# Optimization experiments

Measured on AMD Instinct MI355X. Metric: run time of the kernel, lower is better.

## Reference

```python
import jax, jax.numpy as jnp
import numpy as np

B, N, C, H = 2, 2048, 1024, 16
D = C // H          # head dim = 64
HID = 4 * C         # MLP hidden = 4096
LN_EPS = 1e-5
ROPE_BASE = 10000.0


def layernorm(x, g, b):
    mu = jnp.mean(x, axis=-1, keepdims=True)
    var = jnp.var(x, axis=-1, keepdims=True)
    return (x - mu) * jax.lax.rsqrt(var + LN_EPS) * g + b


def rotate_half(x):
    # interleaved pairs: (x0, x1) -> (-x1, x0), lucidrains rotary_embedding_torch style
    x = x.reshape(*x.shape[:-1], -1, 2)
    x1, x2 = x[..., 0], x[..., 1]
    return jnp.stack([-x2, x1], axis=-1).reshape(*x.shape[:-2], -1)


def rope_cos_sin(n, d, dtype):
    inv_freq = 1.0 / (ROPE_BASE ** (jnp.arange(0, d, 2, dtype=jnp.float32) / d))
    ang = jnp.arange(n, dtype=jnp.float32)[:, None] * inv_freq          # [N, D/2]
    ang = jnp.repeat(ang, 2, axis=-1)                                    # [N, D] interleaved
    return jnp.cos(ang).astype(dtype), jnp.sin(ang).astype(dtype)


def setup_inputs() -> dict:
    key = jax.random.key(0)
    ks = jax.random.split(key, 16)
    s = 0.02
    return {
        "x": jax.random.normal(ks[0], (B, N, C), jnp.float32),
        "ln1_g": jnp.ones((C,), jnp.float32),
        "ln1_b": jnp.zeros((C,), jnp.float32),
        "qkv_w": jax.random.normal(ks[1], (C, 3 * C), jnp.float32) * s,   # stored [in, out]
        "qkv_b": jnp.zeros((3 * C,), jnp.float32),
        "proj_w": jax.random.normal(ks[2], (C, C), jnp.float32) * s,
        "proj_b": jnp.zeros((C,), jnp.float32),
        "ln2_g": jnp.ones((C,), jnp.float32),
        "ln2_b": jnp.zeros((C,), jnp.float32),
        "fc1_w": jax.random.normal(ks[3], (C, HID), jnp.float32) * s,
        "fc1_b": jnp.zeros((HID,), jnp.float32),
        "ffn_ln_g": jnp.ones((HID,), jnp.float32),
        "ffn_ln_b": jnp.zeros((HID,), jnp.float32),
        "fc2_w": jax.random.normal(ks[4], (HID, C), jnp.float32) * s,
        "fc2_b": jnp.zeros((C,), jnp.float32),
    }


def reference(x, ln1_g, ln1_b, qkv_w, qkv_b, proj_w, proj_b,
              ln2_g, ln2_b, fc1_w, fc1_b, ffn_ln_g, ffn_ln_b, fc2_w, fc2_b):
    b, n, c = x.shape
    h, d = H, c // H
    scale = d ** -0.5

    # --- attention branch (pre-norm) ---
    hx = layernorm(x, ln1_g, ln1_b)
    qkv = hx @ qkv_w + qkv_b                                   # [B,N,3C]
    qkv = qkv.reshape(b, n, 3, h, d).transpose(2, 0, 3, 1, 4)  # [3,B,H,N,D]
    q, k, v = qkv[0], qkv[1], qkv[2]

    cos, sin = rope_cos_sin(n, d, x.dtype)                     # [N,D]
    q = q * cos + rotate_half(q) * sin
    k = k * cos + rotate_half(k) * sin

    attn = jax.nn.softmax(jnp.einsum('bhqd,bhkd->bhqk', q, k) * scale, axis=-1)
    o = jnp.einsum('bhqk,bhkd->bhqd', attn, v)                 # [B,H,N,D]
    o = o.transpose(0, 2, 1, 3).reshape(b, n, c)               # B N (H D)
    x = x + o @ proj_w + proj_b

    # --- MLP branch (pre-norm; GELU then LayerNorm on hidden, per FeedForwardBlock) ---
    m = layernorm(x, ln2_g, ln2_b)
    m = jax.nn.gelu(m @ fc1_w + fc1_b, approximate=False)
    m = layernorm(m, ffn_ln_g, ffn_ln_b)
    m = m @ fc2_w + fc2_b
    return x + m
```

## Files before the change

### kernel.cpp

```cpp
#include <hip/hip_runtime.h>
#include <hip/hip_bf16.h>
#include <cmath>

typedef __bf16 bf16_t;
typedef __bf16 bf16x8 __attribute__((ext_vector_type(8)));
typedef float f32x4 __attribute__((ext_vector_type(4)));
typedef float f32x16 __attribute__((ext_vector_type(16)));
typedef unsigned short u16;
typedef unsigned int u32;

#if defined(__has_builtin)
#if __has_builtin(__builtin_amdgcn_exp2f)
#define ATTN_EXP(x) __builtin_amdgcn_exp2f(x)
#define ATTN_LOG2E 1.4426950408889634f
#endif
#endif
#ifndef ATTN_EXP
#define ATTN_EXP(x) __expf(x)
#define ATTN_LOG2E 1.0f
#endif

__device__ __forceinline__ void load16(const bf16_t* g, bf16_t* l) {
  __builtin_amdgcn_global_load_lds((const __attribute__((address_space(1))) u32*)g,
                                   (__attribute__((address_space(3))) u32*)l, 16, 0, 0);
}

__device__ __forceinline__ u32 pk2(float a, float b) {
  bf16_t x = (bf16_t)a, y = (bf16_t)b;
  u16 ux = __builtin_bit_cast(u16, x), uy = __builtin_bit_cast(u16, y);
  return (u32)ux | ((u32)uy << 16);
}

union V4U { u32 w[4]; bf16x8 v; };

__device__ __forceinline__ void tr64(const float* __restrict__ src, bf16_t* __restrict__ dst,
                                     int Kd, int Nd, int ntile, int ktile, int tid) {
  __shared__ float tile[64][68];
  int n0 = ntile * 64, k0 = ktile * 64;
  int r = tid >> 2, c4 = (tid & 3) * 4;
  const float* sp = src + (size_t)(k0 + r) * Nd + n0;
#pragma unroll
  for (int c = 0; c < 4; ++c)
    *(float4*)&tile[r][c * 16 + c4] = *(const float4*)(sp + c * 16 + c4);
  __syncthreads();
  int n = tid >> 2;
  bf16_t* dp = dst + (size_t)(n0 + n) * Kd + k0;
#pragma unroll
  for (int c = 0; c < 4; ++c) {
    int kk = c * 16 + c4;
    uint2 pk;
    pk.x = pk2(tile[kk + 0][n], tile[kk + 1][n]);
    pk.y = pk2(tile[kk + 2][n], tile[kk + 3][n]);
    *(uint2*)(dp + kk) = pk;
  }
}

__global__ __launch_bounds__(256) void prep_kernel(
    const float* __restrict__ qkv_w, const float* __restrict__ proj_w,
    const float* __restrict__ fc1_w, const float* __restrict__ fc2_w,
    bf16_t* __restrict__ qkvT, bf16_t* __restrict__ projT,
    bf16_t* __restrict__ fc1T, bf16_t* __restrict__ fc2T,
    float* __restrict__ ropeC, float* __restrict__ ropeS) {
  int b = blockIdx.x, tid = threadIdx.x;
  if (b < 768) {
    tr64(qkv_w, qkvT, 1024, 3072, b % 48, b / 48, tid);
  } else if (b < 1024) {
    int r = b - 768; tr64(proj_w, projT, 1024, 1024, r % 16, r / 16, tid);
  } else if (b < 2048) {
    int r = b - 1024; tr64(fc1_w, fc1T, 1024, 4096, r % 64, r / 64, tid);
  } else if (b < 3072) {
    int r = b - 2048; tr64(fc2_w, fc2T, 4096, 1024, r % 16, r / 16, tid);
  } else {
    int idx = (b - 3072) * 256 + tid;
    int pos = idx >> 5, t = idx & 31;
    float e = (float)(2 * t) / 64.0f;
    float inv = powf(10000.0f, -e);
    float a = (float)pos * inv;
    ropeC[idx] = cosf(a);
    ropeS[idx] = sinf(a);
  }
}

template <typename TI, int W>
__global__ __launch_bounds__(256) void ln_kernel(const TI* __restrict__ in,
                                                 const float* __restrict__ g,
                                                 const float* __restrict__ b,
                                                 bf16_t* __restrict__ out,
                                                 const float* __restrict__ aux_b,
                                                 float* __restrict__ aux_out) {
  constexpr int CH = (sizeof(TI) == 2) ? 8 : 4;
  constexpr int NS = W / (256 * CH);
  int row = blockIdx.x;
  const TI* p = in + (size_t)row * W;
  float vals[NS * CH];
  float s = 0.f, q = 0.f;
#pragma unroll
  for (int sw = 0; sw < NS; ++sw) {
    int base = sw * (256 * CH) + threadIdx.x * CH;
    if constexpr (sizeof(TI) == 2) {
      bf16x8 v = *(const bf16x8*)(p + base);
#pragma unroll
      for (int e = 0; e < 8; ++e) {
        float f = (float)v[e];
        vals[sw * CH + e] = f; s += f; q += f * f;
      }
    } else {
      float4 v = *(const float4*)(p + base);
      float f0 = v.x, f1 = v.y, f2 = v.z, f3 = v.w;
      vals[sw * CH + 0] = f0; vals[sw * CH + 1] = f1;
      vals[sw * CH + 2] = f2; vals[sw * CH + 3] = f3;
      s += (f0 + f1) + (f2 + f3);
      q += (f0 * f0 + f1 * f1) + (f2 * f2 + f3 * f3);
    }
  }
  for (int off = 32; off; off >>= 1) { s += __shfl_xor(s, off); q += __shfl_xor(q, off); }
  __shared__ float red[8];
  int wave = threadIdx.x >> 6, lane = threadIdx.x & 63;
  if (lane == 0) { red[wave] = s; red[4 + wave] = q; }
  __syncthreads();
  s = red[0] + red[1] + red[2] + red[3];
  q = red[4] + red[5] + red[6] + red[7];
  float mu = s * (1.0f / W);
  float var = q * (1.0f / W) - mu * mu;
  float rstd = rsqrtf(var + 1e-5f);
  bf16_t* op = out + (size_t)row * W;
#pragma unroll
  for (int sw = 0; sw < NS; ++sw) {
    int base = sw * (256 * CH) + threadIdx.x * CH;
    float o[CH];
#pragma unroll
    for (int e = 0; e < CH; ++e)
      o[e] = (vals[sw * CH + e] - mu) * rstd * g[base + e] + b[base + e];
    if constexpr (CH == 8) {
      V4U u;
      u.w[0] = pk2(o[0], o[1]); u.w[1] = pk2(o[2], o[3]);
      u.w[2] = pk2(o[4], o[5]); u.w[3] = pk2(o[6], o[7]);
      *(bf16x8*)(op + base) = u.v;
    } else {
      uint2 pk; pk.x = pk2(o[0], o[1]); pk.y = pk2(o[2], o[3]);
      *(uint2*)(op + base) = pk;
    }
    if (aux_out) {
      float* ap = aux_out + (size_t)row * W + base;
#pragma unroll
      for (int e = 0; e < CH; ++e) ap[e] = vals[sw * CH + e] + aux_b[base + e];
    }
  }
}

enum { EPI_QKV = 0, EPI_RESID = 1, EPI_GELU = 2, EPI_ATOMIC = 3 };

template <int EPI, int TM>
__global__ __launch_bounds__(256, 2) void gemm_bt(
    const bf16_t* __restrict__ A, const bf16_t* __restrict__ Bt, int M, int Nn, int K,
    int gy, int ksteps,
    const float* __restrict__ bias, const float* __restrict__ resid,
    float* __restrict__ outf, bf16_t* __restrict__ outb,
    bf16_t* __restrict__ qb, bf16_t* __restrict__ kb, bf16_t* __restrict__ vtb,
    const float* __restrict__ ropeC, const float* __restrict__ ropeS) {
  constexpr int MT = TM / 32;
  __shared__ bf16_t lsA[2][TM * 32];
  __shared__ bf16_t lsB[2][128 * 32];
  const int tid = threadIdx.x;
  const int lane = tid & 63;
  const int wave = tid >> 6;
  const int l16 = lane & 15, quad = lane >> 4;
  const int wm = (wave >> 1) * (TM / 2), wn = (wave & 1) * 64;
  const int bb = blockIdx.x;
  const int m0 = (bb % gy) * TM, n0 = (bb / gy) * 128;
  const int kbase = blockIdx.y * (ksteps << 5);

  f32x4 acc[MT][4];
  for (int i = 0; i < MT; ++i)
    for (int j = 0; j < 4; ++j) acc[i][j] = {0.f, 0.f, 0.f, 0.f};

  auto stage = [&](int kk, int buf) {
    bf16_t* la = &lsA[buf][0];
    bf16_t* lb = &lsB[buf][0];
#pragma unroll
    for (int i = 0; i < TM / 64; ++i) {
      int s = tid + i * 256;
      int row = s >> 2, ch = (s & 3) ^ (row & 3);
      load16(A + (size_t)(m0 + row) * K + kk + ch * 8, la + s * 8);
    }
#pragma unroll
    for (int i = 0; i < 2; ++i) {
      int s = tid + i * 256;
      int row = s >> 2, ch = (s & 3) ^ (row & 3);
      load16(Bt + (size_t)(n0 + row) * K + kk + ch * 8, lb + s * 8);
    }
  };

  stage(kbase, 0);
  for (int ki = 0; ki < ksteps; ++ki) {
    __syncthreads();
    if (ki + 1 < ksteps) stage(kbase + ((ki + 1) << 5), (ki + 1) & 1);
    const bf16_t* la = &lsA[ki & 1][0];
    const bf16_t* lb = &lsB[ki & 1][0];
    bf16x8 af[MT], bfr[4];
#pragma unroll
    for (int t = 0; t < MT; ++t) {
      int row = wm + t * 16 + l16;
      af[t] = *(const bf16x8*)(la + row * 32 + (quad ^ (row & 3)) * 8);
    }
#pragma unroll
    for (int t = 0; t < 4; ++t) {
      int row = wn + t * 16 + l16;
      bfr[t] = *(const bf16x8*)(lb + row * 32 + (quad ^ (row & 3)) * 8);
    }
#pragma unroll
    for (int mt = 0; mt < MT; ++mt)
#pragma unroll
      for (int nt = 0; nt < 4; ++nt)
        acc[mt][nt] = __builtin_amdgcn_mfma_f32_16x16x32_bf16(af[mt], bfr[nt], acc[mt][nt], 0, 0, 0);
  }

  for (int mt = 0; mt < MT; ++mt) {
    for (int nt = 0; nt < 4; ++nt) {
      int gn = n0 + wn + nt * 16 + l16;
      int gm0 = m0 + wm + mt * 16 + quad * 4;
      if constexpr (EPI == EPI_QKV) {
        int which = gn >> 10;
        int hd = gn & 1023, head = hd >> 6, d = hd & 63;
        if (which == 2) {
          u32 lo, hi;
          {
            float v0 = acc[mt][nt][0] + bias[gn];
            float v1 = acc[mt][nt][1] + bias[gn];
            float v2 = acc[mt][nt][2] + bias[gn];
            float v3 = acc[mt][nt][3] + bias[gn];
            lo = pk2(v0, v1);
            hi = pk2(v2, v3);
          }
          int b = gm0 >> 11, pos = gm0 & 2047;
          int bh = b * 16 + head;
          uint2 pk; pk.x = lo; pk.y = hi;
          *(uint2*)(vtb + ((size_t)bh * 64 + d) * 2048 + pos) = pk;
        } else {
          bf16_t* dst = (which == 0) ? qb : kb;
          int t = d >> 1;
          for (int r = 0; r < 4; ++r) {
            float v = acc[mt][nt][r] + bias[gn];
            float pn = __shfl_xor(v, 1);
            int gm = gm0 + r;
            int b = gm >> 11, pos = gm & 2047;
            float cc = ropeC[pos * 32 + t], ss = ropeS[pos * 32 + t];
            float o = (d & 1) ? (v * cc + pn * ss) : (v * cc - pn * ss);
            dst[(((size_t)(b * 16 + head)) * 2048 + pos) * 64 + d] = (bf16_t)o;
          }
        }
      } else if constexpr (EPI == EPI_GELU) {
        for (int r = 0; r < 4; ++r) {
          int gm = gm0 + r;
          float v = acc[mt][nt][r] + bias[gn];
          float g = 0.5f * v * (1.0f + erff(v * 0.70710678118654752f));
          outb[(size_t)gm * Nn + gn] = (bf16_t)g;
        }
      } else if constexpr (EPI == EPI_ATOMIC) {
        for (int r = 0; r < 4; ++r) {
          int gm = gm0 + r;
          unsafeAtomicAdd(outf + (size_t)gm * Nn + gn, acc[mt][nt][r]);
        }
      } else {
        for (int r = 0; r < 4; ++r) {
          int gm = gm0 + r;
          size_t idx = (size_t)gm * Nn + gn;
          outf[idx] = acc[mt][nt][r] + bias[gn] + resid[idx];
        }
      }
    }
  }
}

__global__ __launch_bounds__(256, 2) void attn_kernel(
    const bf16_t* __restrict__ q, const bf16_t* __restrict__ k,
    const bf16_t* __restrict__ vt, bf16_t* __restrict__ o) {
  __shared__ bf16_t lsK[2][128 * 64];
  __shared__ bf16_t lsV[2][64 * 128];

  const int tid = threadIdx.x, lane = tid & 63, wave = tid >> 6;
  const int c31 = lane & 31, hi = lane >> 5, h7 = c31 & 7;
  const int bh = blockIdx.y, qt = blockIdx.x;
  const int b = bh >> 4, h = bh & 15;
  const bf16_t* qp = q + (size_t)bh * 2048 * 64;
  const bf16_t* kp = k + (size_t)bh * 2048 * 64;
  const bf16_t* vp = vt + (size_t)bh * 64 * 2048;
  const int qrow0 = qt * 128 + wave * 32;
  const int qrow = qrow0 + c31;

  const float QS = 0.125f * ATTN_LOG2E;
  bf16x8 qb[4];
#pragma unroll
  for (int ks = 0; ks < 4; ++ks) {
    bf16x8 t = *(const bf16x8*)(qp + (size_t)qrow * 64 + ks * 16 + hi * 8);
#pragma unroll
    for (int j = 0; j < 8; ++j) t[j] = (bf16_t)((float)t[j] * QS);
    qb[ks] = t;
  }

  f32x16 oacc[2];
  oacc[0] = 0.f; oacc[1] = 0.f;
  float mstate = -3.0e38f, lstate = 0.f;

  auto stage = [&](int kt, int buf) {
    const bf16_t* kg = kp + (size_t)kt * 128 * 64;
    bf16_t* lk = &lsK[buf][0];
    bf16_t* lv = &lsV[buf][0];
#pragma unroll
    for (int i = 0; i < 4; ++i) {
      int s = tid + i * 256;
      int kr = s >> 3, kc = (s & 7) ^ (kr & 7);
      load16(kg + (size_t)kr * 64 + kc * 8, lk + s * 8);
      int vr = s >> 4, vc = (s & 15) ^ (vr & 7);
      load16(vp + (size_t)vr * 2048 + kt * 128 + vc * 8, lv + s * 8);
    }
  };

  stage(0, 0);
  for (int kt = 0; kt < 16; ++kt) {
    __syncthreads();
    if (kt < 15) stage(kt + 1, (kt + 1) & 1);
    const bf16_t* lk = &lsK[kt & 1][0];
    const bf16_t* lv = &lsV[kt & 1][0];

    f32x16 sacc[4];
    sacc[0] = 0.f; sacc[1] = 0.f; sacc[2] = 0.f; sacc[3] = 0.f;
#pragma unroll
    for (int ks = 0; ks < 4; ++ks) {
      int cs = ((ks * 2 + hi) ^ h7) * 8;
#pragma unroll
      for (int nt = 0; nt < 4; ++nt) {
        bf16x8 kf = *(const bf16x8*)(lk + (nt * 32 + c31) * 64 + cs);
        sacc[nt] = __builtin_amdgcn_mfma_f32_32x32x16_bf16(kf, qb[ks], sacc[nt], 0, 0, 0);
      }
    }

    float mx = sacc[0][0];
#pragma unroll
    for (int nt = 0; nt < 4; ++nt)
#pragma unroll
      for (int r = 0; r < 16; ++r) mx = fmaxf(mx, sacc[nt][r]);
    mx = fmaxf(mx, __shfl_xor(mx, 32));
    float mnew = fmaxf(mstate, mx);
    float alpha = ATTN_EXP(mstate - mnew);
    mstate = mnew;
    float rs = 0.f;
    u32 u[4][4][2];
#pragma unroll
    for (int nt = 0; nt < 4; ++nt)
#pragma unroll
      for (int t = 0; t < 4; ++t) {
        float p0 = ATTN_EXP(sacc[nt][4 * t + 0] - mnew);
        float p1 = ATTN_EXP(sacc[nt][4 * t + 1] - mnew);
        float p2 = ATTN_EXP(sacc[nt][4 * t + 2] - mnew);
        float p3 = ATTN_EXP(sacc[nt][4 * t + 3] - mnew);
        rs += (p0 + p1) + (p2 + p3);
        u[nt][t][0] = pk2(p0, p1);
        u[nt][t][1] = pk2(p2, p3);
      }
    rs += __shfl_xor(rs, 32);
    lstate = lstate * alpha + rs;
#pragma unroll
    for (int dt = 0; dt < 2; ++dt)
#pragma unroll
      for (int r = 0; r < 16; ++r) oacc[dt][r] *= alpha;

#pragma unroll
    for (int ks = 0; ks < 8; ++ks) {
      int n = ks >> 1, t0 = (ks & 1) * 2;
      u32 a0 = u[n][t0][0], a1 = u[n][t0][1];
      u32 b0 = u[n][t0 + 1][0], b1 = u[n][t0 + 1][1];
      u32 ax0 = (u32)__shfl_xor((int)a0, 32), ax1 = (u32)__shfl_xor((int)a1, 32);
      u32 bx0 = (u32)__shfl_xor((int)b0, 32), bx1 = (u32)__shfl_xor((int)b1, 32);
      V4U f;
      f.w[0] = hi ? bx0 : a0;
      f.w[1] = hi ? bx1 : a1;
      f.w[2] = hi ? b0 : ax0;
      f.w[3] = hi ? b1 : ax1;
      bf16x8 pf = f.v;
      int cs = ((ks * 2 + hi) ^ h7) * 8;
#pragma unroll
      for (int dt = 0; dt < 2; ++dt) {
        bf16x8 vf = *(const bf16x8*)(lv + (dt * 32 + c31) * 128 + cs);
        oacc[dt] = __builtin_amdgcn_mfma_f32_32x32x16_bf16(vf, pf, oacc[dt], 0, 0, 0);
      }
    }
  }

  float inv = 1.0f / lstate;
  bf16_t* orow = o + ((size_t)(b * 2048 + qrow)) * 1024 + h * 64;
#pragma unroll
  for (int dt = 0; dt < 2; ++dt)
#pragma unroll
    for (int t = 0; t < 4; ++t) {
      int d0 = dt * 32 + 8 * t + 4 * hi;
      uint2 pk;
      pk.x = pk2(oacc[dt][4 * t + 0] * inv, oacc[dt][4 * t + 1] * inv);
      pk.y = pk2(oacc[dt][4 * t + 2] * inv, oacc[dt][4 * t + 3] * inv);
      *(uint2*)(orow + d0) = pk;
    }
}

extern "C" void kernel_launch(void* const* d_in, const int* in_sizes, int n_in,
                              void* d_out, int out_size, void* d_ws, size_t ws_size,
                              hipStream_t stream) {
  const float* x = (const float*)d_in[0];
  const float* ln1_g = (const float*)d_in[1];
  const float* ln1_b = (const float*)d_in[2];
  const float* qkv_w = (const float*)d_in[3];
  const float* qkv_b = (const float*)d_in[4];
  const float* proj_w = (const float*)d_in[5];
  const float* proj_b = (const float*)d_in[6];
  const float* ln2_g = (const float*)d_in[7];
  const float* ln2_b = (const float*)d_in[8];
  const float* fc1_w = (const float*)d_in[9];
  const float* fc1_b = (const float*)d_in[10];
  const float* ffg = (const float*)d_in[11];
  const float* ffb = (const float*)d_in[12];
  const float* fc2_w = (const float*)d_in[13];
  const float* fc2_b = (const float*)d_in[14];
  float* out = (float*)d_out;

  char* ws = (char*)d_ws;
  size_t off = 0;
  auto alloc = [&](size_t n) { char* p = ws + off; off += (n + 255) & ~(size_t)255; return p; };

  bf16_t* qkvT  = (bf16_t*)alloc(3072ull * 1024 * 2);
  bf16_t* projT = (bf16_t*)alloc(1024ull * 1024 * 2);
  bf16_t* fc1T  = (bf16_t*)alloc(4096ull * 1024 * 2);
  bf16_t* fc2T  = (bf16_t*)alloc(1024ull * 4096 * 2);
  float*  ropeC = (float*)alloc(2048ull * 32 * 4);
  float*  ropeS = (float*)alloc(2048ull * 32 * 4);
  bf16_t* hx    = (bf16_t*)alloc(4096ull * 1024 * 2);
  bf16_t* qbuf  = (bf16_t*)alloc(32ull * 2048 * 64 * 2);
  bf16_t* kbuf  = (bf16_t*)alloc(32ull * 2048 * 64 * 2);
  bf16_t* vtbuf = (bf16_t*)alloc(32ull * 64 * 2048 * 2);
  bf16_t* obuf  = (bf16_t*)alloc(4096ull * 1024 * 2);
  float*  x2    = (float*)alloc(4096ull * 1024 * 4);
  bf16_t* h1    = (bf16_t*)alloc(4096ull * 4096 * 2);
  bf16_t* hln   = (bf16_t*)qbuf;

  prep_kernel<<<3328, 256, 0, stream>>>(qkv_w, proj_w, fc1_w, fc2_w,
                                        qkvT, projT, fc1T, fc2T, ropeC, ropeS);

  ln_kernel<float, 1024><<<4096, 256, 0, stream>>>(x, ln1_g, ln1_b, hx, proj_b, x2);
  gemm_bt<EPI_QKV, 128><<<768, 256, 0, stream>>>(hx, qkvT, 4096, 3072, 1024, 32, 32, qkv_b,
      nullptr, nullptr, nullptr, qbuf, kbuf, vtbuf, ropeC, ropeS);
  attn_kernel<<<dim3(16, 32), 256, 0, stream>>>(qbuf, kbuf, vtbuf, obuf);
  gemm_bt<EPI_ATOMIC, 128><<<dim3(256, 2), 256, 0, stream>>>(obuf, projT, 4096, 1024, 1024,
      32, 16, nullptr, nullptr, x2, nullptr, nullptr, nullptr, nullptr, nullptr, nullptr);
  ln_kernel<float, 1024><<<4096, 256, 0, stream>>>(x2, ln2_g, ln2_b, hx, fc2_b, out);
  gemm_bt<EPI_GELU, 128><<<1024, 256, 0, stream>>>(hx, fc1T, 4096, 4096, 1024, 32, 32, fc1_b,
      nullptr, nullptr, h1, nullptr, nullptr, nullptr, nullptr, nullptr);
  ln_kernel<bf16_t, 4096><<<4096, 256, 0, stream>>>(h1, ffg, ffb, hln, nullptr, nullptr);
  gemm_bt<EPI_ATOMIC, 128><<<dim3(256, 4), 256, 0, stream>>>(hln, fc2T, 4096, 1024, 4096,
      32, 32, nullptr, nullptr, out, nullptr, nullptr, nullptr, nullptr, nullptr, nullptr);
}
```

Measured before the change: 417.4 us.

## Replace atomic split-K with partial buffers and reduce; lazy softmax rescale

The proj GEMM now runs without split-K, using a smaller M tile and a fused bias+residual epilogue, instead of atomically accumulating into a pre-seeded x2. The fc2 GEMM writes two split-K partial buffers (reusing the h1 workspace), and a separate reduce kernel sums them with the residual and bias. This removes the atomic traffic and the aux writes in the LayerNorm kernels. The attention softmax also skips the running-max rescale unless the new block max exceeds the old max by more than 8 on some lane. That saves the exp and rescale multiplies but lets probabilities grow to up to 2^8 before normalisation.

Result: faster. 384.4 us (-7.9%).

```diff
diff --git a/kernel.cpp b/kernel.cpp
--- a/kernel.cpp
+++ b/kernel.cpp
@@ -85,9 +85,7 @@
 __global__ __launch_bounds__(256) void ln_kernel(const TI* __restrict__ in,
                                                  const float* __restrict__ g,
                                                  const float* __restrict__ b,
-                                                 bf16_t* __restrict__ out,
-                                                 const float* __restrict__ aux_b,
-                                                 float* __restrict__ aux_out) {
+                                                 bf16_t* __restrict__ out) {
   constexpr int CH = (sizeof(TI) == 2) ? 8 : 4;
   constexpr int NS = W / (256 * CH);
   int row = blockIdx.x;
@@ -140,15 +138,30 @@
       uint2 pk; pk.x = pk2(o[0], o[1]); pk.y = pk2(o[2], o[3]);
       *(uint2*)(op + base) = pk;
     }
-    if (aux_out) {
-      float* ap = aux_out + (size_t)row * W + base;
-#pragma unroll
-      for (int e = 0; e < CH; ++e) ap[e] = vals[sw * CH + e] + aux_b[base + e];
-    }
-  }
-}
-
-enum { EPI_QKV = 0, EPI_RESID = 1, EPI_GELU = 2, EPI_ATOMIC = 3 };
+  }
+}
+
+__global__ __launch_bounds__(256) void reduce2_kernel(
+    const float* __restrict__ part, const float* __restrict__ resid,
+    const float* __restrict__ bias, float* __restrict__ out) {
+  const int total4 = (4096 * 1024) / 4;
+  const float4* p0 = (const float4*)part;
+  const float4* p1 = (const float4*)(part + 4096ull * 1024);
+  const float4* r4 = (const float4*)resid;
+  const float4* b4 = (const float4*)bias;
+  float4* o4 = (float4*)out;
+  for (int i = blockIdx.x * 256 + threadIdx.x; i < total4; i += gridDim.x * 256) {
+    float4 a = p0[i], b = p1[i], r = r4[i], bb = b4[i & 255];
+    float4 o;
+    o.x = (a.x + b.x) + (r.x + bb.x);
+    o.y = (a.y + b.y) + (r.y + bb.y);
+    o.z = (a.z + b.z) + (r.z + bb.z);
+    o.w = (a.w + b.w) + (r.w + bb.w);
+    o4[i] = o;
+  }
+}
+
+enum { EPI_QKV = 0, EPI_RESID = 1, EPI_GELU = 2, EPI_PART = 3 };
 
 template <int EPI, int TM>
 __global__ __launch_bounds__(256, 2) void gemm_bt(
@@ -256,10 +269,11 @@
           float g = 0.5f * v * (1.0f + erff(v * 0.70710678118654752f));
           outb[(size_t)gm * Nn + gn] = (bf16_t)g;
         }
-      } else if constexpr (EPI == EPI_ATOMIC) {
+      } else if constexpr (EPI == EPI_PART) {
+        float* po = outf + (size_t)blockIdx.y * M * Nn;
         for (int r = 0; r < 4; ++r) {
           int gm = gm0 + r;
-          unsafeAtomicAdd(outf + (size_t)gm * Nn + gn, acc[mt][nt][r]);
+          po[(size_t)gm * Nn + gn] = acc[mt][nt][r];
         }
       } else {
         for (int r = 0; r < 4; ++r) {
@@ -341,29 +355,32 @@
 #pragma unroll
       for (int r = 0; r < 16; ++r) mx = fmaxf(mx, sacc[nt][r]);
     mx = fmaxf(mx, __shfl_xor(mx, 32));
-    float mnew = fmaxf(mstate, mx);
-    float alpha = ATTN_EXP(mstate - mnew);
-    mstate = mnew;
+    if (!__all(mx <= mstate + 8.0f)) {
+      float mnew = fmaxf(mstate, mx);
+      float alpha = ATTN_EXP(mstate - mnew);
+      mstate = mnew;
+      lstate *= alpha;
+#pragma unroll
+      for (int dt = 0; dt < 2; ++dt)
+#pragma unroll
+        for (int r = 0; r < 16; ++r) oacc[dt][r] *= alpha;
+    }
     float rs = 0.f;
     u32 u[4][4][2];
 #pragma unroll
     for (int nt = 0; nt < 4; ++nt)
 #pragma unroll
       for (int t = 0; t < 4; ++t) {
-        float p0 = ATTN_EXP(sacc[nt][4 * t + 0] - mnew);
-        float p1 = ATTN_EXP(sacc[nt][4 * t + 1] - mnew);
-        float p2 = ATTN_EXP(sacc[nt][4 * t + 2] - mnew);
-        float p3 = ATTN_EXP(sacc[nt][4 * t + 3] - mnew);
+        float p0 = ATTN_EXP(sacc[nt][4 * t + 0] - mstate);
+        float p1 = ATTN_EXP(sacc[nt][4 * t + 1] - mstate);
+        float p2 = ATTN_EXP(sacc[nt][4 * t + 2] - mstate);
+        float p3 = ATTN_EXP(sacc[nt][4 * t + 3] - mstate);
         rs += (p0 + p1) + (p2 + p3);
         u[nt][t][0] = pk2(p0, p1);
         u[nt][t][1] = pk2(p2, p3);
       }
     rs += __shfl_xor(rs, 32);
-    lstate = lstate * alpha + rs;
-#pragma unroll
-    for (int dt = 0; dt < 2; ++dt)
-#pragma unroll
-      for (int r = 0; r < 16; ++r) oacc[dt][r] *= alpha;
+    lstate += rs;
 
 #pragma unroll
     for (int ks = 0; ks < 8; ++ks) {
@@ -439,20 +456,22 @@
   float*  x2    = (float*)alloc(4096ull * 1024 * 4);
   bf16_t* h1    = (bf16_t*)alloc(4096ull * 4096 * 2);
   bf16_t* hln   = (bf16_t*)qbuf;
+  float*  part  = (float*)h1;
 
   prep_kernel<<<3328, 256, 0, stream>>>(qkv_w, proj_w, fc1_w, fc2_w,
                                         qkvT, projT, fc1T, fc2T, ropeC, ropeS);
 
-  ln_kernel<float, 1024><<<4096, 256, 0, stream>>>(x, ln1_g, ln1_b, hx, proj_b, x2);
+  ln_kernel<float, 1024><<<4096, 256, 0, stream>>>(x, ln1_g, ln1_b, hx);
   gemm_bt<EPI_QKV, 128><<<768, 256, 0, stream>>>(hx, qkvT, 4096, 3072, 1024, 32, 32, qkv_b,
       nullptr, nullptr, nullptr, qbuf, kbuf, vtbuf, ropeC, ropeS);
   attn_kernel<<<dim3(16, 32), 256, 0, stream>>>(qbuf, kbuf, vtbuf, obuf);
-  gemm_bt<EPI_ATOMIC, 128><<<dim3(256, 2), 256, 0, stream>>>(obuf, projT, 4096, 1024, 1024,
-      32, 16, nullptr, nullptr, x2, nullptr, nullptr, nullptr, nullptr, nullptr, nullptr);
-  ln_kernel<float, 1024><<<4096, 256, 0, stream>>>(x2, ln2_g, ln2_b, hx, fc2_b, out);
+  gemm_bt<EPI_RESID, 64><<<512, 256, 0, stream>>>(obuf, projT, 4096, 1024, 1024, 64, 32,
+      proj_b, x, x2, nullptr, nullptr, nullptr, nullptr, nullptr, nullptr);
+  ln_kernel<float, 1024><<<4096, 256, 0, stream>>>(x2, ln2_g, ln2_b, hx);
   gemm_bt<EPI_GELU, 128><<<1024, 256, 0, stream>>>(hx, fc1T, 4096, 4096, 1024, 32, 32, fc1_b,
       nullptr, nullptr, h1, nullptr, nullptr, nullptr, nullptr, nullptr);
-  ln_kernel<bf16_t, 4096><<<4096, 256, 0, stream>>>(h1, ffg, ffb, hln, nullptr, nullptr);
-  gemm_bt<EPI_ATOMIC, 128><<<dim3(256, 4), 256, 0, stream>>>(hln, fc2T, 4096, 1024, 4096,
-      32, 32, nullptr, nullptr, out, nullptr, nullptr, nullptr, nullptr, nullptr, nullptr);
-}
+  ln_kernel<bf16_t, 4096><<<4096, 256, 0, stream>>>(h1, ffg, ffb, hln);
+  gemm_bt<EPI_PART, 128><<<dim3(256, 2), 256, 0, stream>>>(hln, fc2T, 4096, 1024, 4096,
+      32, 64, nullptr, nullptr, part, nullptr, nullptr, nullptr, nullptr, nullptr, nullptr);
+  reduce2_kernel<<<2048, 256, 0, stream>>>(part, x2, fc2_b, out);
+}
```
